# Kernel optimization log

Measured on AMD Instinct MI355X. Metric: run time of the kernel, lower is better.

Reference implementation:

```python
import jax, jax.numpy as jnp
import numpy as np

B, T, C = 2, 2048, 1024
H = 16
DK = C // H


def setup_inputs() -> dict:
    key = jax.random.key(0)
    ks = jax.random.split(key, 5)
    x = jax.random.normal(ks[0], (B, T, C), dtype=jnp.float32)
    # causal mask, broadcastable to [B, H, T, T]; mask==0 -> -inf
    mask = jnp.tril(jnp.ones((T, T), dtype=jnp.int32))[None, None]
    s = 1.0 / np.sqrt(C)
    qkv_w = jax.random.normal(ks[1], (3 * C, C), dtype=jnp.float32) * s  # torch Linear layout [out,in]
    qkv_b = jnp.zeros((3 * C,), dtype=jnp.float32)
    out_w = jax.random.normal(ks[2], (C, C), dtype=jnp.float32) * s
    out_b = jnp.zeros((C,), dtype=jnp.float32)
    return {"x": x, "mask": mask, "qkv_w": qkv_w, "qkv_b": qkv_b,
            "out_w": out_w, "out_b": out_b}


def reference(x, mask, qkv_w, qkv_b, out_w, out_b):
    b, t, c = x.shape
    qkv = x @ qkv_w.T + qkv_b                       # [B,T,3C]
    qkv = qkv.reshape(b, t, 3, H, DK)
    q, k, v = qkv[:, :, 0], qkv[:, :, 1], qkv[:, :, 2]   # [B,T,H,DK]
    scores = jnp.einsum('bqhd,bkhd->bhqk', q, k) / np.sqrt(DK)
    scores = jnp.where(mask == 0, -jnp.inf, scores)
    attn_weights = jax.nn.softmax(scores, axis=-1)       # [B,H,T,T]
    attn_out = jnp.einsum('bhqk,bkhd->bqhd', attn_weights, v).reshape(b, t, c)
    out = attn_out @ out_w.T + out_b
    return out, attn_weights
```

## Files before the change

### kernel.cpp

```cpp
#include <hip/hip_runtime.h>
#include <hip/hip_bf16.h>

typedef short short8  __attribute__((ext_vector_type(8)));
typedef short short4v __attribute__((ext_vector_type(4)));
typedef __bf16 bf16x8 __attribute__((ext_vector_type(8)));
typedef float f32x4   __attribute__((ext_vector_type(4)));
typedef float f32x2   __attribute__((ext_vector_type(2)));

__device__ __forceinline__ void mfma16(f32x4& d, short8 a, short8 b) {
    d = __builtin_amdgcn_mfma_f32_16x16x32_bf16(
            __builtin_bit_cast(bf16x8, a), __builtin_bit_cast(bf16x8, b), d, 0, 0, 0);
}

__device__ __forceinline__ unsigned short f2bf(float f) {
    union { float f; unsigned u; } a; a.f = f;
    unsigned u = a.u;
    return (unsigned short)((u + 0x7fffu + ((u >> 16) & 1u)) >> 16);
}
__device__ __forceinline__ float bf2f(unsigned short us) {
    union { unsigned u; float f; } a; a.u = ((unsigned)us) << 16;
    return a.f;
}

__global__ void cvt_all(const float* __restrict__ x, const float* __restrict__ w1,
                        const float* __restrict__ w2,
                        unsigned short* __restrict__ ox, unsigned short* __restrict__ o1,
                        unsigned short* __restrict__ o2) {
    int i = blockIdx.x * 256 + threadIdx.x;
    const float* src; unsigned short* dst; int j;
    if (i < 1048576)      { src = x;  dst = ox; j = i; }
    else if (i < 1835008) { src = w1; dst = o1; j = i - 1048576; }
    else                  { src = w2; dst = o2; j = i - 1835008; }
    float4 v = ((const float4*)src)[j];
    ushort4 o;
    o.x = f2bf(v.x); o.y = f2bf(v.y); o.z = f2bf(v.z); o.w = f2bf(v.w);
    ((ushort4*)dst)[j] = o;
}

template<int OUTBF, int VTF, int BN>
__global__ __launch_bounds__(256)
void gemm_bt(const unsigned short* __restrict__ A, const unsigned short* __restrict__ Bw,
             const float* __restrict__ bias, void* __restrict__ Cout,
             unsigned short* __restrict__ vt, int M, int N, int K)
{
    constexpr int NN = BN / 32;
    __shared__ unsigned short As[128 * 64];
    __shared__ unsigned short Bs[BN * 64];

    const int tid  = threadIdx.x;
    const int lane = tid & 63;
    const int wid  = tid >> 6;

    const int swz  = (int)((blockIdx.x & 7) * (gridDim.x >> 3) + (blockIdx.x >> 3));
    const int nby  = M >> 7;
    const int row0 = (swz % nby) << 7;
    const int col0 = (swz / nby) * BN;
    const int wr = (wid >> 1) << 6;
    const int wc = (wid & 1) * (BN >> 1);
    const int rl = lane & 15;
    const int g  = lane >> 4;

    f32x4 acc[4][NN] = {};

    for (int k0 = 0; k0 < K; k0 += 64) {
        __syncthreads();
#pragma unroll
        for (int rd = 0; rd < 4; ++rd) {
            int s  = rd * 256 + tid;
            int r  = s >> 3, cs = s & 7;
            int cg = cs ^ (r & 7);
            __builtin_amdgcn_global_load_lds(
                (__attribute__((address_space(1))) void*)(A + (size_t)(row0 + r) * K + k0 + cg * 8),
                (__attribute__((address_space(3))) void*)(As + s * 8), 16, 0, 0);
        }
#pragma unroll
        for (int rd = 0; rd < (BN >> 5); ++rd) {
            int s  = rd * 256 + tid;
            int r  = s >> 3, cs = s & 7;
            int cg = cs ^ (r & 7);
            __builtin_amdgcn_global_load_lds(
                (__attribute__((address_space(1))) void*)(Bw + (size_t)(col0 + r) * K + k0 + cg * 8),
                (__attribute__((address_space(3))) void*)(Bs + s * 8), 16, 0, 0);
        }
        __syncthreads();

#pragma unroll
        for (int h = 0; h < 2; ++h) {
            short8 af[4], bf[NN];
#pragma unroll
            for (int m = 0; m < 4; ++m) {
                int rr = wr + m * 16 + rl;
                int ch = ((h << 2) + g) ^ (rr & 7);
                af[m] = *(const short8*)(As + rr * 64 + ch * 8);
            }
#pragma unroll
            for (int n = 0; n < NN; ++n) {
                int rr = wc + n * 16 + rl;
                int ch = ((h << 2) + g) ^ (rr & 7);
                bf[n] = *(const short8*)(Bs + rr * 64 + ch * 8);
            }
#pragma unroll
            for (int m = 0; m < 4; ++m)
#pragma unroll
                for (int n = 0; n < NN; ++n)
                    mfma16(acc[m][n], af[m], bf[n]);
        }
    }

    const int b  = row0 >> 11;
    const int tg = (row0 & 2047) + wr + (g << 2);
#pragma unroll
    for (int n = 0; n < NN; ++n) {
        int col = col0 + wc + n * 16 + rl;
        float bv = bias[col];
        if (VTF && col >= 2048) {
            int hd = col - 2048;
            unsigned short* vr = vt + ((size_t)((b << 4) + (hd >> 6)) * 64 + (hd & 63)) * 2048;
#pragma unroll
            for (int m = 0; m < 4; ++m) {
                short4v p;
#pragma unroll
                for (int r = 0; r < 4; ++r) p[r] = (short)f2bf(acc[m][n][r] + bv);
                *(short4v*)(vr + tg + m * 16) = p;
            }
        } else {
#pragma unroll
            for (int m = 0; m < 4; ++m) {
#pragma unroll
                for (int r = 0; r < 4; ++r) {
                    int row = row0 + wr + m * 16 + (g << 2) + r;
                    float v = acc[m][n][r] + bv;
                    if (OUTBF) ((unsigned short*)Cout)[(size_t)row * N + col] = f2bf(v);
                    else       __builtin_nontemporal_store(v, (float*)Cout + (size_t)row * N + col);
                }
            }
        }
    }
}

__device__ __forceinline__ int S_addr(int row, int col) {
    return (row << 11) + ((((col >> 3) ^ (row & 7))) << 3) + (col & 7);
}

__global__ __launch_bounds__(256, 2)
void attn_kernel(const unsigned short* __restrict__ qkv,
                 const unsigned short* __restrict__ vt,
                 float* __restrict__ wout,
                 unsigned short* __restrict__ aout)
{
    __shared__ unsigned short Ss[16 * 2048];
    __shared__ float part[4][16];

    const int bid = (int)(((blockIdx.x & 7) << 9) + (blockIdx.x >> 3));
    const int qt = bid & 127;
    const int bh = bid >> 7;
    const int b = bh >> 4, h = bh & 15;
    const int q0 = qt << 4;
    const int tid = threadIdx.x;
    const int wid = tid >> 6;
    const int lane = tid & 63;
    const int rl = lane & 15;
    const int g  = lane >> 4;

    int nt = (qt + 4) & ~3;
    if (nt > 128) nt = 128;
    const int ntiles = nt;
    const int KPAD = ntiles << 4;

    const unsigned short* Qb = qkv + (size_t)((b << 11) + q0) * 3072 + (h << 6);
    short8 qf0 = *(const short8*)(Qb + (size_t)rl * 3072 + g * 8);
    short8 qf1 = *(const short8*)(Qb + (size_t)rl * 3072 + 32 + g * 8);

    const unsigned short* Kb = qkv + (size_t)(b << 11) * 3072 + 1024 + (h << 6);

    float psum[4] = {0.f, 0.f, 0.f, 0.f};

    {
        int kt = wid;
        const unsigned short* kp = Kb + (size_t)(kt * 16 + rl) * 3072;
        short8 ka0 = *(const short8*)(kp + g * 8);
        short8 ka1 = *(const short8*)(kp + 32 + g * 8);
        for (; kt < ntiles; kt += 4) {
            short8 kb0 = ka0, kb1 = ka1;
            if (kt + 4 < ntiles) {
                const unsigned short* kp2 = Kb + (size_t)((kt + 4) * 16 + rl) * 3072;
                kb0 = *(const short8*)(kp2 + g * 8);
                kb1 = *(const short8*)(kp2 + 32 + g * 8);
            }
            f32x4 acc = {};
            __builtin_amdgcn_s_setprio(1);
            mfma16(acc, qf0, ka0);
            mfma16(acc, qf1, ka1);
            __builtin_amdgcn_s_setprio(0);
            int col = kt * 16 + rl;
#pragma unroll
            for (int r = 0; r < 4; ++r) {
                int qrow = g * 4 + r;
                float e = (col <= q0 + qrow) ? __expf(acc[r] * 0.125f) : 0.0f;
                Ss[S_addr(qrow, col)] = f2bf(e);
                psum[r] += e;
            }
            ka0 = kb0; ka1 = kb1;
        }
    }
#pragma unroll
    for (int m = 8; m; m >>= 1)
#pragma unroll
        for (int r = 0; r < 4; ++r) psum[r] += __shfl_xor(psum[r], m);
    if (rl == 0) {
#pragma unroll
        for (int r = 0; r < 4; ++r) part[wid][g * 4 + r] = psum[r];
    }
    __syncthreads();

    f32x4 p0 = {}, p1 = {};
    const unsigned short* vrow = vt + ((size_t)(bh << 6) + wid * 16 + rl) * 2048;
    const int nkc = KPAD >> 5;
    const int wrow = wid + (g << 2);
    const float invw = 1.0f / (part[0][wrow] + part[1][wrow] + part[2][wrow] + part[3][wrow]);
    float* worow = wout + ((size_t)bh * 2048 + q0 + wrow) * 2048;
    const int cb = rl << 1;
    short8 bv = *(const short8*)(vrow + (g << 3));
    for (int ic = 0; ic < 64; ++ic) {
        int colb = (ic << 5) + cb;
        f32x2 o;
        if (ic < nkc) {
            short8 bcur = bv;
            if (ic + 1 < nkc) bv = *(const short8*)(vrow + ((ic + 1) << 5) + (g << 3));
            int c0 = (ic << 2) + g;
            short8 a0 = *(const short8*)(Ss + (rl << 11) + ((c0 ^ (rl & 7)) << 3));
            __builtin_amdgcn_s_setprio(1);
            if (ic & 1) mfma16(p1, a0, bcur); else mfma16(p0, a0, bcur);
            __builtin_amdgcn_s_setprio(0);
            unsigned sv = *(const unsigned*)(Ss + S_addr(wrow, colb));
            o[0] = bf2f((unsigned short)(sv & 0xffffu)) * invw;
            o[1] = bf2f((unsigned short)(sv >> 16)) * invw;
        } else {
            o[0] = 0.f; o[1] = 0.f;
        }
        __builtin_nontemporal_store(o, (f32x2*)(worow + colb));
    }

    f32x4 pacc = p0 + p1;
#pragma unroll
    for (int r = 0; r < 4; ++r) {
        int qrow = g * 4 + r;
        float inv = 1.0f / (part[0][qrow] + part[1][qrow] + part[2][qrow] + part[3][qrow]);
        float v = pacc[r] * inv;
        aout[(size_t)((b << 11) + q0 + qrow) * 1024 + (h << 6) + wid * 16 + rl] = f2bf(v);
    }
}

extern "C" void kernel_launch(void* const* d_in, const int* in_sizes, int n_in,
                              void* d_out, int out_size, void* d_ws, size_t ws_size,
                              hipStream_t stream)
{
    const float* x     = (const float*)d_in[0];
    const float* qkv_w = (const float*)d_in[2];
    const float* qkv_b = (const float*)d_in[3];
    const float* out_w = (const float*)d_in[4];
    const float* out_b = (const float*)d_in[5];

    char* ws = (char*)d_ws;
    unsigned short* xbf   = (unsigned short*)(ws);
    unsigned short* wqkv  = (unsigned short*)(ws + 8388608);
    unsigned short* woutw = (unsigned short*)(ws + 14680064);
    unsigned short* qkv   = (unsigned short*)(ws + 16777216);
    unsigned short* vt    = (unsigned short*)(ws + 41943040);
    unsigned short* aout  = (unsigned short*)(ws + 50331648);

    float* out  = (float*)d_out;
    float* wout = (float*)d_out + 4194304;

    cvt_all<<<8192, 256, 0, stream>>>(x, qkv_w, out_w, xbf, wqkv, woutw);

    gemm_bt<1, 1, 128><<<768, 256, 0, stream>>>(xbf, wqkv, qkv_b, qkv, vt, 4096, 3072, 1024);
    attn_kernel<<<4096, 256, 0, stream>>>(qkv, vt, wout, aout);
    gemm_bt<0, 0, 64><<<512, 256, 0, stream>>>(aout, woutw, out_b, out, nullptr, 4096, 1024, 1024);
}
```

Before: 237.2 us.

## Split QKV output into head-major K buffer and packed Q, widen attention stores

The QKV GEMM epilogue now writes K into a per-(batch,head) contiguous [T,64] buffer and Q into a compact [B*T,1024] buffer, so attention K-tile loads read dense 128-byte rows instead of striding across a 3072-wide row. The attention kernel deepens K prefetch to two tiles ahead and processes 64 keys per PV iteration with two MFMAs, writing the attention weight matrix with 16-byte nontemporal stores instead of 8-byte ones. The output projection GEMM moves to 64x64 tiles with 1024 blocks and uses ordinary stores instead of nontemporal ones. The K epilogue does scalar strided 2-byte stores, which may cost some bandwidth in the GEMM, and more registers are held live for the deeper prefetch.

Measured after the change: 211.6 us. 1.12x faster.

```diff
diff --git a/kernel.cpp b/kernel.cpp
--- a/kernel.cpp
+++ b/kernel.cpp
@@ -5,7 +5,6 @@
 typedef short short4v __attribute__((ext_vector_type(4)));
 typedef __bf16 bf16x8 __attribute__((ext_vector_type(8)));
 typedef float f32x4   __attribute__((ext_vector_type(4)));
-typedef float f32x2   __attribute__((ext_vector_type(2)));
 
 __device__ __forceinline__ void mfma16(f32x4& d, short8 a, short8 b) {
     d = __builtin_amdgcn_mfma_f32_16x16x32_bf16(
@@ -37,14 +36,16 @@
     ((ushort4*)dst)[j] = o;
 }
 
-template<int OUTBF, int VTF, int BN>
+template<int OUTBF, int VTF, int BM, int BN>
 __global__ __launch_bounds__(256)
 void gemm_bt(const unsigned short* __restrict__ A, const unsigned short* __restrict__ Bw,
              const float* __restrict__ bias, void* __restrict__ Cout,
-             unsigned short* __restrict__ vt, int M, int N, int K)
+             unsigned short* __restrict__ vt, unsigned short* __restrict__ khb,
+             int M, int N, int K)
 {
+    constexpr int MM = BM / 32;
     constexpr int NN = BN / 32;
-    __shared__ unsigned short As[128 * 64];
+    __shared__ unsigned short As[BM * 64];
     __shared__ unsigned short Bs[BN * 64];
 
     const int tid  = threadIdx.x;
@@ -52,20 +53,20 @@
     const int wid  = tid >> 6;
 
     const int swz  = (int)((blockIdx.x & 7) * (gridDim.x >> 3) + (blockIdx.x >> 3));
-    const int nby  = M >> 7;
-    const int row0 = (swz % nby) << 7;
+    const int nby  = M / BM;
+    const int row0 = (swz % nby) * BM;
     const int col0 = (swz / nby) * BN;
-    const int wr = (wid >> 1) << 6;
+    const int wr = (wid >> 1) * (BM >> 1);
     const int wc = (wid & 1) * (BN >> 1);
     const int rl = lane & 15;
     const int g  = lane >> 4;
 
-    f32x4 acc[4][NN] = {};
+    f32x4 acc[MM][NN] = {};
 
     for (int k0 = 0; k0 < K; k0 += 64) {
         __syncthreads();
 #pragma unroll
-        for (int rd = 0; rd < 4; ++rd) {
+        for (int rd = 0; rd < (BM >> 5); ++rd) {
             int s  = rd * 256 + tid;
             int r  = s >> 3, cs = s & 7;
             int cg = cs ^ (r & 7);
@@ -86,9 +87,9 @@
 
 #pragma unroll
         for (int h = 0; h < 2; ++h) {
-            short8 af[4], bf[NN];
-#pragma unroll
-            for (int m = 0; m < 4; ++m) {
+            short8 af[MM], bf[NN];
+#pragma unroll
+            for (int m = 0; m < MM; ++m) {
                 int rr = wr + m * 16 + rl;
                 int ch = ((h << 2) + g) ^ (rr & 7);
                 af[m] = *(const short8*)(As + rr * 64 + ch * 8);
@@ -100,7 +101,7 @@
                 bf[n] = *(const short8*)(Bs + rr * 64 + ch * 8);
             }
 #pragma unroll
-            for (int m = 0; m < 4; ++m)
+            for (int m = 0; m < MM; ++m)
 #pragma unroll
                 for (int n = 0; n < NN; ++n)
                     mfma16(acc[m][n], af[m], bf[n]);
@@ -117,21 +118,36 @@
             int hd = col - 2048;
             unsigned short* vr = vt + ((size_t)((b << 4) + (hd >> 6)) * 64 + (hd & 63)) * 2048;
 #pragma unroll
-            for (int m = 0; m < 4; ++m) {
+            for (int m = 0; m < MM; ++m) {
                 short4v p;
 #pragma unroll
                 for (int r = 0; r < 4; ++r) p[r] = (short)f2bf(acc[m][n][r] + bv);
                 *(short4v*)(vr + tg + m * 16) = p;
             }
+        } else if (VTF && col >= 1024) {
+            int hd = col - 1024;
+            unsigned short* kr = khb + ((size_t)((b << 4) + (hd >> 6)) << 17) + (hd & 63);
+#pragma unroll
+            for (int m = 0; m < MM; ++m)
+#pragma unroll
+                for (int r = 0; r < 4; ++r)
+                    kr[(size_t)(tg + m * 16 + r) << 6] = f2bf(acc[m][n][r] + bv);
+        } else if (VTF) {
+#pragma unroll
+            for (int m = 0; m < MM; ++m)
+#pragma unroll
+                for (int r = 0; r < 4; ++r)
+                    ((unsigned short*)Cout)[(size_t)(row0 + wr + m * 16 + (g << 2) + r) * 1024 + col]
+                        = f2bf(acc[m][n][r] + bv);
         } else {
 #pragma unroll
-            for (int m = 0; m < 4; ++m) {
+            for (int m = 0; m < MM; ++m) {
 #pragma unroll
                 for (int r = 0; r < 4; ++r) {
                     int row = row0 + wr + m * 16 + (g << 2) + r;
                     float v = acc[m][n][r] + bv;
                     if (OUTBF) ((unsigned short*)Cout)[(size_t)row * N + col] = f2bf(v);
-                    else       __builtin_nontemporal_store(v, (float*)Cout + (size_t)row * N + col);
+                    else       ((float*)Cout)[(size_t)row * N + col] = v;
                 }
             }
         }
@@ -143,7 +159,8 @@
 }
 
 __global__ __launch_bounds__(256, 2)
-void attn_kernel(const unsigned short* __restrict__ qkv,
+void attn_kernel(const unsigned short* __restrict__ qbuf,
+                 const unsigned short* __restrict__ khb,
                  const unsigned short* __restrict__ vt,
                  float* __restrict__ wout,
                  unsigned short* __restrict__ aout)
@@ -167,30 +184,38 @@
     const int ntiles = nt;
     const int KPAD = ntiles << 4;
 
-    const unsigned short* Qb = qkv + (size_t)((b << 11) + q0) * 3072 + (h << 6);
-    short8 qf0 = *(const short8*)(Qb + (size_t)rl * 3072 + g * 8);
-    short8 qf1 = *(const short8*)(Qb + (size_t)rl * 3072 + 32 + g * 8);
-
-    const unsigned short* Kb = qkv + (size_t)(b << 11) * 3072 + 1024 + (h << 6);
+    const unsigned short* Qb = qbuf + (size_t)((b << 11) + q0) * 1024 + (h << 6);
+    short8 qf0 = *(const short8*)(Qb + rl * 1024 + g * 8);
+    short8 qf1 = *(const short8*)(Qb + rl * 1024 + 32 + g * 8);
+
+    const unsigned short* Kh = khb + ((size_t)bh << 17);
 
     float psum[4] = {0.f, 0.f, 0.f, 0.f};
 
     {
-        int kt = wid;
-        const unsigned short* kp = Kb + (size_t)(kt * 16 + rl) * 3072;
-        short8 ka0 = *(const short8*)(kp + g * 8);
-        short8 ka1 = *(const short8*)(kp + 32 + g * 8);
-        for (; kt < ntiles; kt += 4) {
-            short8 kb0 = ka0, kb1 = ka1;
-            if (kt + 4 < ntiles) {
-                const unsigned short* kp2 = Kb + (size_t)((kt + 4) * 16 + rl) * 3072;
+        short8 ka0, ka1, kb0, kb1;
+        {
+            const unsigned short* kp = Kh + (size_t)((wid * 16 + rl) << 6);
+            ka0 = *(const short8*)(kp + g * 8);
+            ka1 = *(const short8*)(kp + 32 + g * 8);
+        }
+        if (wid + 4 < ntiles) {
+            const unsigned short* kp = Kh + (size_t)((((wid + 4) * 16) + rl) << 6);
+            kb0 = *(const short8*)(kp + g * 8);
+            kb1 = *(const short8*)(kp + 32 + g * 8);
+        } else { kb0 = ka0; kb1 = ka1; }
+        for (int kt = wid; kt < ntiles; kt += 4) {
+            short8 kc0 = ka0, kc1 = ka1;
+            ka0 = kb0; ka1 = kb1;
+            if (kt + 8 < ntiles) {
+                const unsigned short* kp2 = Kh + (size_t)((((kt + 8) * 16) + rl) << 6);
                 kb0 = *(const short8*)(kp2 + g * 8);
                 kb1 = *(const short8*)(kp2 + 32 + g * 8);
             }
             f32x4 acc = {};
             __builtin_amdgcn_s_setprio(1);
-            mfma16(acc, qf0, ka0);
-            mfma16(acc, qf1, ka1);
+            mfma16(acc, qf0, kc0);
+            mfma16(acc, qf1, kc1);
             __builtin_amdgcn_s_setprio(0);
             int col = kt * 16 + rl;
 #pragma unroll
@@ -200,7 +225,6 @@
                 Ss[S_addr(qrow, col)] = f2bf(e);
                 psum[r] += e;
             }
-            ka0 = kb0; ka1 = kb1;
         }
     }
 #pragma unroll
@@ -215,30 +239,37 @@
 
     f32x4 p0 = {}, p1 = {};
     const unsigned short* vrow = vt + ((size_t)(bh << 6) + wid * 16 + rl) * 2048;
-    const int nkc = KPAD >> 5;
+    const int np = KPAD >> 6;
     const int wrow = wid + (g << 2);
     const float invw = 1.0f / (part[0][wrow] + part[1][wrow] + part[2][wrow] + part[3][wrow]);
     float* worow = wout + ((size_t)bh * 2048 + q0 + wrow) * 2048;
-    const int cb = rl << 1;
-    short8 bv = *(const short8*)(vrow + (g << 3));
-    for (int ic = 0; ic < 64; ++ic) {
-        int colb = (ic << 5) + cb;
-        f32x2 o;
-        if (ic < nkc) {
-            short8 bcur = bv;
-            if (ic + 1 < nkc) bv = *(const short8*)(vrow + ((ic + 1) << 5) + (g << 3));
-            int c0 = (ic << 2) + g;
-            short8 a0 = *(const short8*)(Ss + (rl << 11) + ((c0 ^ (rl & 7)) << 3));
+    short8 bv0 = *(const short8*)(vrow + (g << 3));
+    short8 bv1 = *(const short8*)(vrow + 32 + (g << 3));
+    for (int ic = 0; ic < 32; ++ic) {
+        int colb = (ic << 6) + (rl << 2);
+        f32x4 o;
+        if (ic < np) {
+            short8 c0 = bv0, c1 = bv1;
+            if (ic + 1 < np) {
+                bv0 = *(const short8*)(vrow + ((ic + 1) << 6) + (g << 3));
+                bv1 = *(const short8*)(vrow + ((ic + 1) << 6) + 32 + (g << 3));
+            }
+            int k0c = (ic << 3) + g;
+            short8 a0 = *(const short8*)(Ss + (rl << 11) + ((k0c ^ (rl & 7)) << 3));
+            short8 a1 = *(const short8*)(Ss + (rl << 11) + (((k0c + 4) ^ (rl & 7)) << 3));
             __builtin_amdgcn_s_setprio(1);
-            if (ic & 1) mfma16(p1, a0, bcur); else mfma16(p0, a0, bcur);
+            mfma16(p0, a0, c0);
+            mfma16(p1, a1, c1);
             __builtin_amdgcn_s_setprio(0);
-            unsigned sv = *(const unsigned*)(Ss + S_addr(wrow, colb));
-            o[0] = bf2f((unsigned short)(sv & 0xffffu)) * invw;
-            o[1] = bf2f((unsigned short)(sv >> 16)) * invw;
+            short4v sv = *(const short4v*)(Ss + S_addr(wrow, colb));
+            o[0] = bf2f((unsigned short)sv[0]) * invw;
+            o[1] = bf2f((unsigned short)sv[1]) * invw;
+            o[2] = bf2f((unsigned short)sv[2]) * invw;
+            o[3] = bf2f((unsigned short)sv[3]) * invw;
         } else {
-            o[0] = 0.f; o[1] = 0.f;
-        }
-        __builtin_nontemporal_store(o, (f32x2*)(worow + colb));
+            o[0] = 0.f; o[1] = 0.f; o[2] = 0.f; o[3] = 0.f;
+        }
+        __builtin_nontemporal_store(o, (f32x4*)(worow + colb));
     }
 
     f32x4 pacc = p0 + p1;
@@ -265,16 +296,17 @@
     unsigned short* xbf   = (unsigned short*)(ws);
     unsigned short* wqkv  = (unsigned short*)(ws + 8388608);
     unsigned short* woutw = (unsigned short*)(ws + 14680064);
-    unsigned short* qkv   = (unsigned short*)(ws + 16777216);
-    unsigned short* vt    = (unsigned short*)(ws + 41943040);
-    unsigned short* aout  = (unsigned short*)(ws + 50331648);
+    unsigned short* qbuf  = (unsigned short*)(ws + 16777216);
+    unsigned short* vt    = (unsigned short*)(ws + 25165824);
+    unsigned short* aout  = (unsigned short*)(ws + 33554432);
+    unsigned short* khb   = (unsigned short*)(ws + 41943040);
 
     float* out  = (float*)d_out;
     float* wout = (float*)d_out + 4194304;
 
     cvt_all<<<8192, 256, 0, stream>>>(x, qkv_w, out_w, xbf, wqkv, woutw);
 
-    gemm_bt<1, 1, 128><<<768, 256, 0, stream>>>(xbf, wqkv, qkv_b, qkv, vt, 4096, 3072, 1024);
-    attn_kernel<<<4096, 256, 0, stream>>>(qkv, vt, wout, aout);
-    gemm_bt<0, 0, 64><<<512, 256, 0, stream>>>(aout, woutw, out_b, out, nullptr, 4096, 1024, 1024);
-}
+    gemm_bt<1, 1, 128, 128><<<768, 256, 0, stream>>>(xbf, wqkv, qkv_b, qbuf, vt, khb, 4096, 3072, 1024);
+    attn_kernel<<<4096, 256, 0, stream>>>(qbuf, khb, vt, wout, aout);
+    gemm_bt<0, 0, 64, 64><<<1024, 256, 0, stream>>>(aout, woutw, out_b, out, nullptr, nullptr, 4096, 1024, 1024);
+}
```
